# Performance work log

Hardware: AMD Instinct MI355X
Metric: run time of the kernel (lower is better)

## Reference

```python
import jax, jax.numpy as jnp
import numpy as np

N = 100000
NEG_SLOPE = 0.2
EPS = 1e-16


def gat_conv(x, src, dst, W, a_src, a_dst, bias, heads, out_ch, concat):
    # add self loops (PyG default add_self_loops=True)
    loop = jnp.arange(N, dtype=src.dtype)
    src = jnp.concatenate([src, loop])
    dst = jnp.concatenate([dst, loop])

    h = (x @ W).reshape(N, heads, out_ch)            # [N,H,C]
    alpha_s = (h * a_src).sum(-1)                    # [N,H]
    alpha_d = (h * a_dst).sum(-1)                    # [N,H]
    e = jax.nn.leaky_relu(alpha_s[src] + alpha_d[dst], NEG_SLOPE)  # [E,H]
    # segment softmax over destination-node neighborhoods
    m = jax.lax.stop_gradient(jax.ops.segment_max(e, dst, num_segments=N))
    ee = jnp.exp(e - m[dst])
    denom = jax.ops.segment_sum(ee, dst, num_segments=N)
    w = ee / (denom[dst] + EPS)                      # [E,H]
    out = jax.ops.segment_sum(h[src] * w[:, :, None], dst, num_segments=N)  # [N,H,C]
    if concat:
        out = out.reshape(N, heads * out_ch)
    else:
        out = out.mean(axis=1)
    return out + bias


def setup_inputs() -> dict:
    key = jax.random.key(0)
    ks = jax.random.split(key, 12)
    in_dim, hid, heads, out_dim = 128, 32, 4, 128
    E = 1600000
    x = jax.random.normal(ks[0], (N, in_dim), dtype=jnp.float32)
    edge_index = jax.random.randint(ks[1], (2, E), 0, N, dtype=jnp.int32)
    s1 = 1.0 / np.sqrt(in_dim)
    W1 = jax.random.uniform(ks[2], (in_dim, heads * hid), minval=-s1, maxval=s1, dtype=jnp.float32)
    a_src1 = jax.random.normal(ks[3], (heads, hid), dtype=jnp.float32) * 0.1
    a_dst1 = jax.random.normal(ks[4], (heads, hid), dtype=jnp.float32) * 0.1
    b1 = jnp.zeros((heads * hid,), dtype=jnp.float32)
    s2 = 1.0 / np.sqrt(heads * hid)
    W2 = jax.random.uniform(ks[5], (heads * hid, out_dim), minval=-s2, maxval=s2, dtype=jnp.float32)
    a_src2 = jax.random.normal(ks[6], (1, out_dim), dtype=jnp.float32) * 0.1
    a_dst2 = jax.random.normal(ks[7], (1, out_dim), dtype=jnp.float32) * 0.1
    b2 = jnp.zeros((out_dim,), dtype=jnp.float32)
    return {"x": x, "edge_index": edge_index, "W1": W1, "a_src1": a_src1,
            "a_dst1": a_dst1, "b1": b1, "W2": W2, "a_src2": a_src2,
            "a_dst2": a_dst2, "b2": b2}


def reference(x, edge_index, W1, a_src1, a_dst1, b1, W2, a_src2, a_dst2, b2):
    src, dst = edge_index[0], edge_index[1]
    h = gat_conv(x, src, dst, W1, a_src1, a_dst1, b1, heads=4, out_ch=32, concat=True)
    h = jax.nn.elu(h)
    # dropout is identity in eval mode
    out = gat_conv(h, src, dst, W2, a_src2, a_dst2, b2, heads=1, out_ch=128, concat=False)
    return out
```

## Files before the change

kernel.cpp:

```cpp
#include <hip/hip_runtime.h>
#include <hip/hip_fp16.h>
#include <math.h>

#define NEG_SLOPE 0.2f

__device__ __forceinline__ float lrelu(float x) { return x >= 0.f ? x : NEG_SLOPE * x; }


__global__ void hist_kernel(const int* __restrict__ dst, int E, int* __restrict__ cnt) {
    int i = blockIdx.x * blockDim.x + threadIdx.x;
    int stride = gridDim.x * blockDim.x;
    for (; i < E; i += stride) atomicAdd(&cnt[dst[i]], 1);
}

__global__ void alloc_kernel(const int* __restrict__ cnt, int N,
                             int* __restrict__ start, int* __restrict__ total) {
    int i = blockIdx.x * blockDim.x + threadIdx.x;
    int lane = threadIdx.x & 63;
    int v = (i < N) ? cnt[i] + 1 : 0;
    int incl = v;
#pragma unroll
    for (int d = 1; d < 64; d <<= 1) {
        int t = __shfl_up(incl, d);
        if (lane >= d) incl += t;
    }
    int wtot = __shfl(incl, 63);
    int base = 0;
    if (lane == 0) base = atomicAdd(total, wtot);
    base = __shfl(base, 0);
    if (i < N) start[i] = base + incl - v;
}

__global__ void scatter_kernel(const int* __restrict__ src, const int* __restrict__ dst,
                               int E, int N, const int* __restrict__ start,
                               int* __restrict__ fill, int* __restrict__ col) {
    int i = blockIdx.x * blockDim.x + threadIdx.x;
    int stride = gridDim.x * blockDim.x;
    int tot = E + N;
    for (; i < tot; i += stride) {
        int s, d;
        if (i < E) { s = src[i]; d = dst[i]; }
        else       { s = i - E; d = s; }
        int p = start[d] + atomicAdd(&fill[d], 1);
        col[p] = s;
    }
}


template <int H>
__global__ __launch_bounds__(256) void gemm_tiled_kernel(
    const float* __restrict__ X, const float* __restrict__ W,
    const float* __restrict__ avs, const float* __restrict__ avd,
    __half* __restrict__ HmH, float* __restrict__ As, float* __restrict__ Ad, int N) {
    __shared__ float Xs[32][64];
    __shared__ float Ws[32][128];
    const int tid = threadIdx.x;
    const int tx = tid & 31;
    const int ty = tid >> 5;
    const int row0 = blockIdx.x * 64;

    float acc[8][4];
#pragma unroll
    for (int r = 0; r < 8; ++r)
#pragma unroll
        for (int c = 0; c < 4; ++c) acc[r][c] = 0.f;

    const float4 as_v = *(const float4*)(avs + tx * 4);
    const float4 ad_v = *(const float4*)(avd + tx * 4);

    for (int k0 = 0; k0 < 128; k0 += 32) {
#pragma unroll
        for (int i = 0; i < 2; ++i) {
            int c = tid + 256 * i;
            int r = c & 63;
            int kc = (c >> 6) << 2;
            int grow = row0 + r;
            float4 v = make_float4(0.f, 0.f, 0.f, 0.f);
            if (grow < N) v = *(const float4*)(X + (size_t)grow * 128 + k0 + kc);
            Xs[kc + 0][r] = v.x;
            Xs[kc + 1][r] = v.y;
            Xs[kc + 2][r] = v.z;
            Xs[kc + 3][r] = v.w;
        }
#pragma unroll
        for (int i = 0; i < 4; ++i) {
            int c = tid + 256 * i;
            int kk = c >> 5;
            int cc = (c & 31) << 2;
            *(float4*)(&Ws[kk][cc]) = *(const float4*)(W + (size_t)(k0 + kk) * 128 + cc);
        }
        __syncthreads();
#pragma unroll
        for (int k = 0; k < 32; ++k) {
            float4 xa = *(const float4*)(&Xs[k][ty * 8]);
            float4 xb = *(const float4*)(&Xs[k][ty * 8 + 4]);
            float4 wv = *(const float4*)(&Ws[k][tx * 4]);
            float xf[8] = {xa.x, xa.y, xa.z, xa.w, xb.x, xb.y, xb.z, xb.w};
            float wf[4] = {wv.x, wv.y, wv.z, wv.w};
#pragma unroll
            for (int r = 0; r < 8; ++r)
#pragma unroll
                for (int c = 0; c < 4; ++c) acc[r][c] += xf[r] * wf[c];
        }
        __syncthreads();
    }

#pragma unroll
    for (int r = 0; r < 8; ++r) {
        int grow = row0 + ty * 8 + r;
        if (grow >= N) continue;
        float4 o = make_float4(acc[r][0], acc[r][1], acc[r][2], acc[r][3]);
        __half2* o2 = (__half2*)(HmH + (size_t)grow * 128 + tx * 4);
        o2[0] = __floats2half2_rn(o.x, o.y);
        o2[1] = __floats2half2_rn(o.z, o.w);
        float ps = o.x * as_v.x + o.y * as_v.y + o.z * as_v.z + o.w * as_v.w;
        float pd = o.x * ad_v.x + o.y * ad_v.y + o.z * ad_v.z + o.w * ad_v.w;
        if (H == 4) {
            ps += __shfl_xor(ps, 1); ps += __shfl_xor(ps, 2); ps += __shfl_xor(ps, 4);
            pd += __shfl_xor(pd, 1); pd += __shfl_xor(pd, 2); pd += __shfl_xor(pd, 4);
            if ((tx & 7) == 0) {
                int h = tx >> 3;
                As[(size_t)grow * 4 + h] = ps;
                Ad[(size_t)grow * 4 + h] = pd;
            }
        } else {
#pragma unroll
            for (int m = 1; m <= 16; m <<= 1) {
                ps += __shfl_xor(ps, m);
                pd += __shfl_xor(pd, m);
            }
            if (tx == 0) { As[grow] = ps; Ad[grow] = pd; }
        }
    }
}


__global__ __launch_bounds__(256) void agg1_kernel(
    const float4* __restrict__ Hm4,
    const int* __restrict__ col,
    const int* __restrict__ start, const int* __restrict__ cnt,
    const float4* __restrict__ As4, const float4* __restrict__ Ad4,
    const float* __restrict__ bias, float* __restrict__ G, int N) {
    const int lane = threadIdx.x & 63;
    const int node = (blockIdx.x * 256 + threadIdx.x) >> 6;
    if (node >= N) return;
    const int qid = lane >> 4;
    const int l15 = lane & 15;
    const int head = l15 >> 2;
    const int s = start[node];
    const int e_end = s + cnt[node] + 1;
    const float4 ad4 = Ad4[node];
    const float adh = head == 0 ? ad4.x : head == 1 ? ad4.y : head == 2 ? ad4.z : ad4.w;

    float acc[8];
#pragma unroll
    for (int c = 0; c < 8; ++c) acc[c] = 0.f;
    float dacc = 0.f;

    for (int j = s; j < e_end; j += 4) {
        const int jj = j + qid;
        const bool act = jj < e_end;
        const int u = act ? col[jj] : 0;
        const float4 a4 = As4[u];
        const float ah = head == 0 ? a4.x : head == 1 ? a4.y : head == 2 ? a4.z : a4.w;
        const float p = act ? __expf(lrelu(ah + adh)) : 0.f;
        dacc += p;
        const float4 hv = Hm4[(size_t)u * 16 + l15];
        const __half2* h2 = (const __half2*)&hv;
        const float2 f0 = __half22float2(h2[0]);
        const float2 f1 = __half22float2(h2[1]);
        const float2 f2 = __half22float2(h2[2]);
        const float2 f3 = __half22float2(h2[3]);
        acc[0] += p * f0.x; acc[1] += p * f0.y;
        acc[2] += p * f1.x; acc[3] += p * f1.y;
        acc[4] += p * f2.x; acc[5] += p * f2.y;
        acc[6] += p * f3.x; acc[7] += p * f3.y;
    }

    dacc += __shfl_xor(dacc, 1);
    dacc += __shfl_xor(dacc, 2);
    dacc += __shfl_xor(dacc, 16);
    dacc += __shfl_xor(dacc, 32);
    const float iv = 1.f / (dacc * 0.25f + 1e-16f);

#pragma unroll
    for (int c = 0; c < 8; ++c) {
        acc[c] += __shfl_xor(acc[c], 16);
        acc[c] += __shfl_xor(acc[c], 32);
    }

    if (qid == 0) {
        const float4 b0 = ((const float4*)bias)[l15 * 2];
        const float4 b1 = ((const float4*)bias)[l15 * 2 + 1];
        float o[8];
        o[0] = acc[0] * iv + b0.x; o[1] = acc[1] * iv + b0.y;
        o[2] = acc[2] * iv + b0.z; o[3] = acc[3] * iv + b0.w;
        o[4] = acc[4] * iv + b1.x; o[5] = acc[5] * iv + b1.y;
        o[6] = acc[6] * iv + b1.z; o[7] = acc[7] * iv + b1.w;
#pragma unroll
        for (int c = 0; c < 8; ++c) o[c] = o[c] > 0.f ? o[c] : expm1f(o[c]);
        float4* dst = (float4*)(G + (size_t)node * 128 + l15 * 8);
        dst[0] = make_float4(o[0], o[1], o[2], o[3]);
        dst[1] = make_float4(o[4], o[5], o[6], o[7]);
    }
}


__global__ __launch_bounds__(256) void agg2_kernel(
    const float4* __restrict__ Hm4, const int* __restrict__ col,
    const int* __restrict__ start, const int* __restrict__ cnt,
    const float* __restrict__ As, const float* __restrict__ Ad,
    const float* __restrict__ bias, float* __restrict__ Out, int N) {
    const int lane = threadIdx.x & 63;
    const int node = (blockIdx.x * 256 + threadIdx.x) >> 6;
    if (node >= N) return;
    const int qid = lane >> 4;
    const int l15 = lane & 15;
    const int s = start[node];
    const int e_end = s + cnt[node] + 1;
    const float adh = Ad[node];

    float acc[8];
#pragma unroll
    for (int c = 0; c < 8; ++c) acc[c] = 0.f;
    float dacc = 0.f;

    for (int j = s; j < e_end; j += 4) {
        const int jj = j + qid;
        const bool act = jj < e_end;
        const int u = act ? col[jj] : 0;
        const float a = As[u];
        const float p = act ? __expf(lrelu(a + adh)) : 0.f;
        dacc += p;
        const float4 hv = Hm4[(size_t)u * 16 + l15];
        const __half2* h2 = (const __half2*)&hv;
        const float2 f0 = __half22float2(h2[0]);
        const float2 f1 = __half22float2(h2[1]);
        const float2 f2 = __half22float2(h2[2]);
        const float2 f3 = __half22float2(h2[3]);
        acc[0] += p * f0.x; acc[1] += p * f0.y;
        acc[2] += p * f1.x; acc[3] += p * f1.y;
        acc[4] += p * f2.x; acc[5] += p * f2.y;
        acc[6] += p * f3.x; acc[7] += p * f3.y;
    }

#pragma unroll
    for (int m = 1; m <= 32; m <<= 1) dacc += __shfl_xor(dacc, m);
    const float iv = 1.f / (dacc * 0.0625f + 1e-16f);

#pragma unroll
    for (int c = 0; c < 8; ++c) {
        acc[c] += __shfl_xor(acc[c], 16);
        acc[c] += __shfl_xor(acc[c], 32);
    }

    if (qid == 0) {
        const float4 b0 = ((const float4*)bias)[l15 * 2];
        const float4 b1 = ((const float4*)bias)[l15 * 2 + 1];
        float4* dst = (float4*)(Out + (size_t)node * 128 + l15 * 8);
        dst[0] = make_float4(acc[0] * iv + b0.x, acc[1] * iv + b0.y,
                             acc[2] * iv + b0.z, acc[3] * iv + b0.w);
        dst[1] = make_float4(acc[4] * iv + b1.x, acc[5] * iv + b1.y,
                             acc[6] * iv + b1.z, acc[7] * iv + b1.w);
    }
}


static inline size_t align256(size_t x) { return (x + 255) & ~(size_t)255; }

extern "C" void kernel_launch(void* const* d_in, const int* in_sizes, int n_in,
                              void* d_out, int out_size, void* d_ws, size_t ws_size,
                              hipStream_t stream) {
    const float* x = (const float*)d_in[0];
    const int* edge_index = (const int*)d_in[1];
    const float* W1 = (const float*)d_in[2];
    const float* a_src1 = (const float*)d_in[3];
    const float* a_dst1 = (const float*)d_in[4];
    const float* b1 = (const float*)d_in[5];
    const float* W2 = (const float*)d_in[6];
    const float* a_src2 = (const float*)d_in[7];
    const float* a_dst2 = (const float*)d_in[8];
    const float* b2 = (const float*)d_in[9];

    const int N = in_sizes[0] / 128;
    const int E = in_sizes[1] / 2;
    const int* src = edge_index;
    const int* dst = edge_index + E;

    char* ws = (char*)d_ws;
    size_t off = 0;
    int* cnt = (int*)(ws + off);   off += align256((size_t)N * 4);
    int* fill = (int*)(ws + off);  off += align256((size_t)N * 4);
    int* total = (int*)(ws + off); off += 256;
    size_t zero_bytes = off;
    int* start = (int*)(ws + off); off += align256((size_t)N * 4);
    int* col = (int*)(ws + off);   off += align256((size_t)(E + N) * 4);
    float* As1 = (float*)(ws + off); off += align256((size_t)N * 16);
    float* Ad1 = (float*)(ws + off); off += align256((size_t)N * 16);
    float* As2 = (float*)(ws + off); off += align256((size_t)N * 4);
    float* Ad2 = (float*)(ws + off); off += align256((size_t)N * 4);
    __half* HmH = (__half*)(ws + off); off += align256((size_t)N * 128 * 2);
    float* bufB = (float*)d_out;
    (void)ws_size;

    hipMemsetAsync(d_ws, 0, zero_bytes, stream);

    hist_kernel<<<2048, 256, 0, stream>>>(dst, E, cnt);
    alloc_kernel<<<(N + 255) / 256, 256, 0, stream>>>(cnt, N, start, total);
    scatter_kernel<<<2048, 256, 0, stream>>>(src, dst, E, N, start, fill, col);

    const int gtiles = (N + 63) / 64;

    gemm_tiled_kernel<4><<<gtiles, 256, 0, stream>>>(x, W1, a_src1, a_dst1, HmH, As1, Ad1, N);
    agg1_kernel<<<(N + 3) / 4, 256, 0, stream>>>((const float4*)HmH, col, start, cnt,
                                                 (const float4*)As1, (const float4*)Ad1,
                                                 b1, bufB, N);

    gemm_tiled_kernel<1><<<gtiles, 256, 0, stream>>>(bufB, W2, a_src2, a_dst2, HmH, As2, Ad2, N);
    agg2_kernel<<<(N + 3) / 4, 256, 0, stream>>>((const float4*)HmH, col, start, cnt,
                                                 As2, Ad2, b2, (float*)d_out, N);
}
```

Before: 606.7 us.

## Record per-edge rank during histogram and widen aggregation to 8 edges per step

```diff
diff --git a/kernel.cpp b/kernel.cpp
--- a/kernel.cpp
+++ b/kernel.cpp
@@ -6,11 +6,10 @@
 
 __device__ __forceinline__ float lrelu(float x) { return x >= 0.f ? x : NEG_SLOPE * x; }
 
-
-__global__ void hist_kernel(const int* __restrict__ dst, int E, int* __restrict__ cnt) {
+__global__ void hist_rank_kernel(const int* __restrict__ dst, int E,
+                                 int* __restrict__ cnt, int* __restrict__ rank) {
     int i = blockIdx.x * blockDim.x + threadIdx.x;
-    int stride = gridDim.x * blockDim.x;
-    for (; i < E; i += stride) atomicAdd(&cnt[dst[i]], 1);
+    if (i < E) rank[i] = atomicAdd(&cnt[dst[i]], 1);
 }
 
 __global__ void alloc_kernel(const int* __restrict__ cnt, int N,
@@ -32,17 +31,16 @@
 }
 
 __global__ void scatter_kernel(const int* __restrict__ src, const int* __restrict__ dst,
-                               int E, int N, const int* __restrict__ start,
-                               int* __restrict__ fill, int* __restrict__ col) {
+                               const int* __restrict__ rank, const int* __restrict__ cnt,
+                               const int* __restrict__ start, int E, int N,
+                               int* __restrict__ col) {
     int i = blockIdx.x * blockDim.x + threadIdx.x;
-    int stride = gridDim.x * blockDim.x;
-    int tot = E + N;
-    for (; i < tot; i += stride) {
-        int s, d;
-        if (i < E) { s = src[i]; d = dst[i]; }
-        else       { s = i - E; d = s; }
-        int p = start[d] + atomicAdd(&fill[d], 1);
-        col[p] = s;
+    if (i < E) {
+        int d = dst[i];
+        col[start[d] + rank[i]] = src[i];
+    } else if (i < E + N) {
+        int n = i - E;
+        col[start[n] + cnt[n]] = n;
     }
 }
 
@@ -144,64 +142,82 @@
     const int lane = threadIdx.x & 63;
     const int node = (blockIdx.x * 256 + threadIdx.x) >> 6;
     if (node >= N) return;
-    const int qid = lane >> 4;
-    const int l15 = lane & 15;
-    const int head = l15 >> 2;
+    const int qid = lane >> 3;
+    const int l7 = lane & 7;
+    const int hA = l7 >> 2;
     const int s = start[node];
     const int e_end = s + cnt[node] + 1;
     const float4 ad4 = Ad4[node];
-    const float adh = head == 0 ? ad4.x : head == 1 ? ad4.y : head == 2 ? ad4.z : ad4.w;
-
-    float acc[8];
-#pragma unroll
-    for (int c = 0; c < 8; ++c) acc[c] = 0.f;
-    float dacc = 0.f;
-
-    for (int j = s; j < e_end; j += 4) {
+    const float adA = hA == 0 ? ad4.x : ad4.y;
+    const float adB = hA == 0 ? ad4.z : ad4.w;
+
+    float accA[8], accB[8];
+#pragma unroll
+    for (int c = 0; c < 8; ++c) { accA[c] = 0.f; accB[c] = 0.f; }
+    float dA = 0.f, dB = 0.f;
+
+    for (int j = s; j < e_end; j += 8) {
         const int jj = j + qid;
         const bool act = jj < e_end;
         const int u = act ? col[jj] : 0;
         const float4 a4 = As4[u];
-        const float ah = head == 0 ? a4.x : head == 1 ? a4.y : head == 2 ? a4.z : a4.w;
-        const float p = act ? __expf(lrelu(ah + adh)) : 0.f;
-        dacc += p;
-        const float4 hv = Hm4[(size_t)u * 16 + l15];
-        const __half2* h2 = (const __half2*)&hv;
-        const float2 f0 = __half22float2(h2[0]);
-        const float2 f1 = __half22float2(h2[1]);
-        const float2 f2 = __half22float2(h2[2]);
-        const float2 f3 = __half22float2(h2[3]);
-        acc[0] += p * f0.x; acc[1] += p * f0.y;
-        acc[2] += p * f1.x; acc[3] += p * f1.y;
-        acc[4] += p * f2.x; acc[5] += p * f2.y;
-        acc[6] += p * f3.x; acc[7] += p * f3.y;
-    }
-
-    dacc += __shfl_xor(dacc, 1);
-    dacc += __shfl_xor(dacc, 2);
-    dacc += __shfl_xor(dacc, 16);
-    dacc += __shfl_xor(dacc, 32);
-    const float iv = 1.f / (dacc * 0.25f + 1e-16f);
+        const float aA = hA == 0 ? a4.x : a4.y;
+        const float aB = hA == 0 ? a4.z : a4.w;
+        const float pA = act ? __expf(lrelu(aA + adA)) : 0.f;
+        const float pB = act ? __expf(lrelu(aB + adB)) : 0.f;
+        dA += pA; dB += pB;
+        const float4 hvA = Hm4[(size_t)u * 16 + l7];
+        const float4 hvB = Hm4[(size_t)u * 16 + 8 + l7];
+        const __half2* cA = (const __half2*)&hvA;
+        const __half2* cB = (const __half2*)&hvB;
+#pragma unroll
+        for (int q = 0; q < 4; ++q) {
+            float2 fa = __half22float2(cA[q]);
+            float2 fb = __half22float2(cB[q]);
+            accA[2 * q] += pA * fa.x; accA[2 * q + 1] += pA * fa.y;
+            accB[2 * q] += pB * fb.x; accB[2 * q + 1] += pB * fb.y;
+        }
+    }
+
+#pragma unroll
+    for (int m = 0; m < 5; ++m) {
+        const int msk = (int[]){1, 2, 8, 16, 32}[m];
+        dA += __shfl_xor(dA, msk);
+        dB += __shfl_xor(dB, msk);
+    }
+    const float ivA = 1.f / (dA * 0.25f + 1e-16f);
+    const float ivB = 1.f / (dB * 0.25f + 1e-16f);
 
 #pragma unroll
     for (int c = 0; c < 8; ++c) {
-        acc[c] += __shfl_xor(acc[c], 16);
-        acc[c] += __shfl_xor(acc[c], 32);
+        accA[c] += __shfl_xor(accA[c], 8);
+        accA[c] += __shfl_xor(accA[c], 16);
+        accA[c] += __shfl_xor(accA[c], 32);
+        accB[c] += __shfl_xor(accB[c], 8);
+        accB[c] += __shfl_xor(accB[c], 16);
+        accB[c] += __shfl_xor(accB[c], 32);
     }
 
     if (qid == 0) {
-        const float4 b0 = ((const float4*)bias)[l15 * 2];
-        const float4 b1 = ((const float4*)bias)[l15 * 2 + 1];
-        float o[8];
-        o[0] = acc[0] * iv + b0.x; o[1] = acc[1] * iv + b0.y;
-        o[2] = acc[2] * iv + b0.z; o[3] = acc[3] * iv + b0.w;
-        o[4] = acc[4] * iv + b1.x; o[5] = acc[5] * iv + b1.y;
-        o[6] = acc[6] * iv + b1.z; o[7] = acc[7] * iv + b1.w;
-#pragma unroll
-        for (int c = 0; c < 8; ++c) o[c] = o[c] > 0.f ? o[c] : expm1f(o[c]);
-        float4* dst = (float4*)(G + (size_t)node * 128 + l15 * 8);
-        dst[0] = make_float4(o[0], o[1], o[2], o[3]);
-        dst[1] = make_float4(o[4], o[5], o[6], o[7]);
+        const float4* b4 = (const float4*)bias;
+        const float4 bA0 = b4[2 * l7],      bA1 = b4[2 * l7 + 1];
+        const float4 bB0 = b4[16 + 2 * l7], bB1 = b4[17 + 2 * l7];
+        float o[16];
+        o[0] = accA[0] * ivA + bA0.x; o[1] = accA[1] * ivA + bA0.y;
+        o[2] = accA[2] * ivA + bA0.z; o[3] = accA[3] * ivA + bA0.w;
+        o[4] = accA[4] * ivA + bA1.x; o[5] = accA[5] * ivA + bA1.y;
+        o[6] = accA[6] * ivA + bA1.z; o[7] = accA[7] * ivA + bA1.w;
+        o[8] = accB[0] * ivB + bB0.x; o[9] = accB[1] * ivB + bB0.y;
+        o[10] = accB[2] * ivB + bB0.z; o[11] = accB[3] * ivB + bB0.w;
+        o[12] = accB[4] * ivB + bB1.x; o[13] = accB[5] * ivB + bB1.y;
+        o[14] = accB[6] * ivB + bB1.z; o[15] = accB[7] * ivB + bB1.w;
+#pragma unroll
+        for (int c = 0; c < 16; ++c) o[c] = o[c] > 0.f ? o[c] : expm1f(o[c]);
+        float4* dst = (float4*)G + (size_t)node * 32;
+        dst[2 * l7]      = make_float4(o[0], o[1], o[2], o[3]);
+        dst[2 * l7 + 1]  = make_float4(o[4], o[5], o[6], o[7]);
+        dst[16 + 2 * l7] = make_float4(o[8], o[9], o[10], o[11]);
+        dst[17 + 2 * l7] = make_float4(o[12], o[13], o[14], o[15]);
     }
 }
 
@@ -214,54 +230,63 @@
     const int lane = threadIdx.x & 63;
     const int node = (blockIdx.x * 256 + threadIdx.x) >> 6;
     if (node >= N) return;
-    const int qid = lane >> 4;
-    const int l15 = lane & 15;
+    const int qid = lane >> 3;
+    const int l7 = lane & 7;
     const int s = start[node];
     const int e_end = s + cnt[node] + 1;
     const float adh = Ad[node];
 
-    float acc[8];
-#pragma unroll
-    for (int c = 0; c < 8; ++c) acc[c] = 0.f;
+    float accA[8], accB[8];
+#pragma unroll
+    for (int c = 0; c < 8; ++c) { accA[c] = 0.f; accB[c] = 0.f; }
     float dacc = 0.f;
 
-    for (int j = s; j < e_end; j += 4) {
+    for (int j = s; j < e_end; j += 8) {
         const int jj = j + qid;
         const bool act = jj < e_end;
         const int u = act ? col[jj] : 0;
-        const float a = As[u];
-        const float p = act ? __expf(lrelu(a + adh)) : 0.f;
+        const float p = act ? __expf(lrelu(As[u] + adh)) : 0.f;
         dacc += p;
-        const float4 hv = Hm4[(size_t)u * 16 + l15];
-        const __half2* h2 = (const __half2*)&hv;
-        const float2 f0 = __half22float2(h2[0]);
-        const float2 f1 = __half22float2(h2[1]);
-        const float2 f2 = __half22float2(h2[2]);
-        const float2 f3 = __half22float2(h2[3]);
-        acc[0] += p * f0.x; acc[1] += p * f0.y;
-        acc[2] += p * f1.x; acc[3] += p * f1.y;
-        acc[4] += p * f2.x; acc[5] += p * f2.y;
-        acc[6] += p * f3.x; acc[7] += p * f3.y;
+        const float4 hvA = Hm4[(size_t)u * 16 + l7];
+        const float4 hvB = Hm4[(size_t)u * 16 + 8 + l7];
+        const __half2* cA = (const __half2*)&hvA;
+        const __half2* cB = (const __half2*)&hvB;
+#pragma unroll
+        for (int q = 0; q < 4; ++q) {
+            float2 fa = __half22float2(cA[q]);
+            float2 fb = __half22float2(cB[q]);
+            accA[2 * q] += p * fa.x; accA[2 * q + 1] += p * fa.y;
+            accB[2 * q] += p * fb.x; accB[2 * q + 1] += p * fb.y;
+        }
     }
 
 #pragma unroll
     for (int m = 1; m <= 32; m <<= 1) dacc += __shfl_xor(dacc, m);
-    const float iv = 1.f / (dacc * 0.0625f + 1e-16f);
+    const float iv = 1.f / (dacc * 0.125f + 1e-16f);
 
 #pragma unroll
     for (int c = 0; c < 8; ++c) {
-        acc[c] += __shfl_xor(acc[c], 16);
-        acc[c] += __shfl_xor(acc[c], 32);
+        accA[c] += __shfl_xor(accA[c], 8);
+        accA[c] += __shfl_xor(accA[c], 16);
+        accA[c] += __shfl_xor(accA[c], 32);
+        accB[c] += __shfl_xor(accB[c], 8);
+        accB[c] += __shfl_xor(accB[c], 16);
+        accB[c] += __shfl_xor(accB[c], 32);
     }
 
     if (qid == 0) {
-        const float4 b0 = ((const float4*)bias)[l15 * 2];
-        const float4 b1 = ((const float4*)bias)[l15 * 2 + 1];
-        float4* dst = (float4*)(Out + (size_t)node * 128 + l15 * 8);
-        dst[0] = make_float4(acc[0] * iv + b0.x, acc[1] * iv + b0.y,
-                             acc[2] * iv + b0.z, acc[3] * iv + b0.w);
-        dst[1] = make_float4(acc[4] * iv + b1.x, acc[5] * iv + b1.y,
-                             acc[6] * iv + b1.z, acc[7] * iv + b1.w);
+        const float4* b4 = (const float4*)bias;
+        const float4 bA0 = b4[2 * l7],      bA1 = b4[2 * l7 + 1];
+        const float4 bB0 = b4[16 + 2 * l7], bB1 = b4[17 + 2 * l7];
+        float4* dst = (float4*)Out + (size_t)node * 32;
+        dst[2 * l7] = make_float4(accA[0] * iv + bA0.x, accA[1] * iv + bA0.y,
+                                  accA[2] * iv + bA0.z, accA[3] * iv + bA0.w);
+        dst[2 * l7 + 1] = make_float4(accA[4] * iv + bA1.x, accA[5] * iv + bA1.y,
+                                      accA[6] * iv + bA1.z, accA[7] * iv + bA1.w);
+        dst[16 + 2 * l7] = make_float4(accB[0] * iv + bB0.x, accB[1] * iv + bB0.y,
+                                       accB[2] * iv + bB0.z, accB[3] * iv + bB0.w);
+        dst[17 + 2 * l7] = make_float4(accB[4] * iv + bB1.x, accB[5] * iv + bB1.y,
+                                       accB[6] * iv + bB1.z, accB[7] * iv + bB1.w);
     }
 }
 
@@ -290,10 +315,10 @@
     char* ws = (char*)d_ws;
     size_t off = 0;
     int* cnt = (int*)(ws + off);   off += align256((size_t)N * 4);
-    int* fill = (int*)(ws + off);  off += align256((size_t)N * 4);
     int* total = (int*)(ws + off); off += 256;
     size_t zero_bytes = off;
     int* start = (int*)(ws + off); off += align256((size_t)N * 4);
+    int* rank = (int*)(ws + off);  off += align256((size_t)E * 4);
     int* col = (int*)(ws + off);   off += align256((size_t)(E + N) * 4);
     float* As1 = (float*)(ws + off); off += align256((size_t)N * 16);
     float* Ad1 = (float*)(ws + off); off += align256((size_t)N * 16);
@@ -305,9 +330,10 @@
 
     hipMemsetAsync(d_ws, 0, zero_bytes, stream);
 
-    hist_kernel<<<2048, 256, 0, stream>>>(dst, E, cnt);
+    hist_rank_kernel<<<(E + 255) / 256, 256, 0, stream>>>(dst, E, cnt, rank);
     alloc_kernel<<<(N + 255) / 256, 256, 0, stream>>>(cnt, N, start, total);
-    scatter_kernel<<<2048, 256, 0, stream>>>(src, dst, E, N, start, fill, col);
+    scatter_kernel<<<(E + N + 255) / 256, 256, 0, stream>>>(src, dst, rank, cnt, start,
+                                                            E, N, col);
 
     const int gtiles = (N + 63) / 64;
 
```

After: 506.8 us. 16.5% less time.
